# Performance work log

Measured on AMD Instinct MI355X. Metric: run time of the kernel, lower is better.

Reference implementation:

```python
import jax, jax.numpy as jnp
import numpy as np

D_MODEL = 256
D_FF = 2048
H_HEADS = 8
N_LEVELS = 5
N_POINTS = 4
SPATIAL = [(128, 128), (64, 64), (32, 32), (16, 16), (8, 8)]
LV = sum(h * w for h, w in SPATIAL)  # 21824
LQ = 900
B = 8
D_HEAD = D_MODEL // H_HEADS


def _layer_norm(x, g, b, eps=1e-5):
    m = jnp.mean(x, -1, keepdims=True)
    v = jnp.mean((x - m) ** 2, -1, keepdims=True)
    return (x - m) * jax.lax.rsqrt(v + eps) * g + b


def _ms_deform_core(value, loc, attn_w):
    # value [B,Lv,H,D]; loc [B,Lq,H,L,P,2] normalized in [0,1]; attn_w [B,Lq,H,L,P]
    Bn, Lq = loc.shape[0], loc.shape[1]
    Dh = value.shape[-1]
    out = jnp.zeros((Bn, H_HEADS, Lq, Dh), value.dtype)
    start = 0
    for l, (Hh, Ww) in enumerate(SPATIAL):
        v = value[:, start:start + Hh * Ww].transpose(0, 2, 1, 3)  # [B,H,HW,D]
        start += Hh * Ww
        xy = loc[:, :, :, l]  # [B,Lq,H,P,2]
        # grid_sample align_corners=False: pixel = norm*size - 0.5
        x = xy[..., 0] * Ww - 0.5
        y = xy[..., 1] * Hh - 0.5
        x0 = jnp.floor(x); y0 = jnp.floor(y)
        fx = x - x0; fy = y - y0
        samp = jnp.zeros((Bn, H_HEADS, Lq * N_POINTS, Dh), value.dtype)
        corners = ((0, 0, (1 - fx) * (1 - fy)), (1, 0, fx * (1 - fy)),
                   (0, 1, (1 - fx) * fy), (1, 1, fx * fy))
        for dx, dy, wgt in corners:
            xc = x0 + dx; yc = y0 + dy
            valid = (xc >= 0) & (xc < Ww) & (yc >= 0) & (yc < Hh)  # zero padding
            idx = (jnp.clip(yc, 0, Hh - 1) * Ww + jnp.clip(xc, 0, Ww - 1)).astype(jnp.int32)
            wv = jnp.where(valid, wgt, 0.0)
            idx_r = idx.transpose(0, 2, 1, 3).reshape(Bn, H_HEADS, Lq * N_POINTS)
            wv_r = wv.transpose(0, 2, 1, 3).reshape(Bn, H_HEADS, Lq * N_POINTS)
            g = jnp.take_along_axis(v, idx_r[..., None], axis=2)  # [B,H,LqP,D]
            samp = samp + wv_r[..., None] * g
        samp = samp.reshape(Bn, H_HEADS, Lq, N_POINTS, Dh)
        aw = attn_w[:, :, :, l].transpose(0, 2, 1, 3)  # [B,H,Lq,P]
        out = out + (samp * aw[..., None]).sum(axis=3)
    return out.transpose(0, 2, 1, 3).reshape(Bn, Lq, H_HEADS * Dh)


def _forward(tgt, tgt_query_pos, tgt_reference_points, memory,
             sa_w_q, sa_b_q, sa_w_k, sa_b_k, sa_w_v, sa_b_v, sa_w_o, sa_b_o,
             ca_w_off, ca_b_off, ca_w_attn, ca_b_attn, ca_w_val, ca_b_val, ca_w_out, ca_b_out,
             ffn_w1, ffn_b1, ffn_w2, ffn_b2,
             ln1_g, ln1_b, ln2_g, ln2_b, ln3_g, ln3_b):
    Lq, Bn, C = tgt.shape
    scale = float(1.0 / np.sqrt(D_HEAD))
    # ---- self-attention (torch nn.MultiheadAttention, seq-first) ----
    qk = tgt + tgt_query_pos
    def heads(x):
        return x.reshape(Lq, Bn, H_HEADS, D_HEAD).transpose(1, 2, 0, 3)
    q = heads(qk @ sa_w_q + sa_b_q) * scale
    k = heads(qk @ sa_w_k + sa_b_k)
    v = heads(tgt @ sa_w_v + sa_b_v)
    attn = jax.nn.softmax(jnp.einsum('bhqd,bhkd->bhqk', q, k), axis=-1)
    o = jnp.einsum('bhqk,bhkd->bhqd', attn, v).transpose(2, 0, 1, 3).reshape(Lq, Bn, C)
    tgt = _layer_norm(tgt + (o @ sa_w_o + sa_b_o), ln2_g, ln2_b)
    # ---- multi-scale deformable cross-attention ----
    qb = (tgt + tgt_query_pos).transpose(1, 0, 2)            # [B,Lq,C]
    ref = tgt_reference_points.transpose(1, 0, 2, 3)         # [B,Lq,L,2]
    value = (memory.transpose(1, 0, 2) @ ca_w_val + ca_b_val).reshape(Bn, LV, H_HEADS, D_HEAD)
    off = (qb @ ca_w_off + ca_b_off).reshape(Bn, Lq, H_HEADS, N_LEVELS, N_POINTS, 2)
    aw = jax.nn.softmax((qb @ ca_w_attn + ca_b_attn).reshape(Bn, Lq, H_HEADS, N_LEVELS * N_POINTS), axis=-1)
    aw = aw.reshape(Bn, Lq, H_HEADS, N_LEVELS, N_POINTS)
    offset_normalizer = jnp.asarray([[w, h] for h, w in SPATIAL], tgt.dtype)  # (W,H) per level
    loc = ref[:, :, None, :, None, :] + off / offset_normalizer[None, None, None, :, None, :]
    samp = _ms_deform_core(value, loc, aw)                   # [B,Lq,C]
    o = (samp @ ca_w_out + ca_b_out).transpose(1, 0, 2)
    tgt = _layer_norm(tgt + o, ln1_g, ln1_b)
    # ---- FFN ----
    h = jax.nn.relu(tgt @ ffn_w1 + ffn_b1)
    tgt = _layer_norm(tgt + (h @ ffn_w2 + ffn_b2), ln3_g, ln3_b)
    return tgt


def setup_inputs() -> dict:
    key = jax.random.key(0)
    ks = iter(jax.random.split(key, 64))
    f32 = jnp.float32
    def nrm(shape, s=1.0):
        return (s * jax.random.normal(next(ks), shape)).astype(f32)
    inp = {}
    inp['tgt'] = nrm((LQ, B, D_MODEL))
    inp['tgt_query_pos'] = nrm((LQ, B, D_MODEL))
    inp['tgt_reference_points'] = jax.random.uniform(next(ks), (LQ, B, N_LEVELS, 2), f32)
    inp['memory'] = nrm((LV, B, D_MODEL))
    inp['memory_spatial_shapes'] = jnp.asarray(SPATIAL, jnp.int32)
    inp['memory_level_start_index'] = jnp.asarray(np.cumsum([0] + [h * w for h, w in SPATIAL[:-1]]), jnp.int32)
    for n, shp in [('sa_w_q', (D_MODEL, D_MODEL)), ('sa_w_k', (D_MODEL, D_MODEL)),
                   ('sa_w_v', (D_MODEL, D_MODEL)), ('sa_w_o', (D_MODEL, D_MODEL)),
                   ('ca_w_off', (D_MODEL, H_HEADS * N_LEVELS * N_POINTS * 2)),
                   ('ca_w_attn', (D_MODEL, H_HEADS * N_LEVELS * N_POINTS)),
                   ('ca_w_val', (D_MODEL, D_MODEL)), ('ca_w_out', (D_MODEL, D_MODEL)),
                   ('ffn_w1', (D_MODEL, D_FF)), ('ffn_w2', (D_FF, D_MODEL))]:
        inp[n] = nrm(shp, 0.02)
    for n, d in [('sa_b_q', D_MODEL), ('sa_b_k', D_MODEL), ('sa_b_v', D_MODEL), ('sa_b_o', D_MODEL),
                 ('ca_b_off', H_HEADS * N_LEVELS * N_POINTS * 2), ('ca_b_attn', H_HEADS * N_LEVELS * N_POINTS),
                 ('ca_b_val', D_MODEL), ('ca_b_out', D_MODEL), ('ffn_b1', D_FF), ('ffn_b2', D_MODEL)]:
        inp[n] = jnp.zeros((d,), f32)
    for n in ['ln1', 'ln2', 'ln3']:
        inp[n + '_g'] = jnp.ones((D_MODEL,), f32)
        inp[n + '_b'] = jnp.zeros((D_MODEL,), f32)
    return inp


def reference(tgt, tgt_query_pos, tgt_reference_points, memory,
              memory_spatial_shapes, memory_level_start_index,
              sa_w_q, sa_b_q, sa_w_k, sa_b_k, sa_w_v, sa_b_v, sa_w_o, sa_b_o,
              ca_w_off, ca_b_off, ca_w_attn, ca_b_attn, ca_w_val, ca_b_val, ca_w_out, ca_b_out,
              ffn_w1, ffn_b1, ffn_w2, ffn_b2,
              ln1_g, ln1_b, ln2_g, ln2_b, ln3_g, ln3_b):
    # spatial shapes / level start index are static metadata (SPATIAL), kept for API parity
    return _forward(tgt, tgt_query_pos, tgt_reference_points, memory,
                    sa_w_q, sa_b_q, sa_w_k, sa_b_k, sa_w_v, sa_b_v, sa_w_o, sa_b_o,
                    ca_w_off, ca_b_off, ca_w_attn, ca_b_attn, ca_w_val, ca_b_val, ca_w_out, ca_b_out,
                    ffn_w1, ffn_b1, ffn_w2, ffn_b2,
                    ln1_g, ln1_b, ln2_g, ln2_b, ln3_g, ln3_b)
```

## Files before the change

kernel.cpp:

```cpp
#include <hip/hip_runtime.h>
#include <hip/hip_bf16.h>
#include <type_traits>

#define LQ    900
#define BSZ   8
#define ROWS  (LQ*BSZ)
#define CDIM  256
#define QKS   512
#define OAS   480
#define NH    8
#define DH    32
#define LVTOT 21824
#define VROWS (LVTOT*BSZ)
#define DFF   2048

typedef unsigned short u16;
typedef short short8 __attribute__((ext_vector_type(8)));
typedef float f32x4 __attribute__((ext_vector_type(4)));

__device__ __forceinline__ u16 f2bf(float f) {
    __hip_bfloat16 h = __float2bfloat16(f);
    return *reinterpret_cast<u16*>(&h);
}

#define SWZ(r) (((r) & 3) ^ (((r) >> 2) & 3))
#define ATTN_SCALE 0.1767766952966369f

struct PrepArgs {
    const float* Wq; const float* Wk; const float* Wv; const float* Wo;
    const float* Wval; const float* Wout; const float* Woff; const float* Watt;
    const float* W1; const float* W2;
    u16* WqkT; u16* WvT; u16* WoT; u16* WvalT; u16* WoutT; u16* WoaT; u16* W1T; u16* W2T;
    const float* bq; const float* bk; const float* boff; const float* batt;
    float* bqk; float* boa;
};
__global__ __launch_bounds__(256) void prep_kernel(PrepArgs a) {
    __shared__ float t[32][33];
    const int id = blockIdx.x;
    if (id == 1528) {
        const int tx = threadIdx.x;
        if (tx < 256) { a.bqk[tx] = a.bq[tx] * ATTN_SCALE; a.bqk[256 + tx] = a.bk[tx]; }
        for (int i = tx; i < 320; i += 256) a.boa[i] = a.boff[i];
        if (tx < 160) a.boa[320 + tx] = a.batt[tx];
        return;
    }
    const float* W; u16* Wt; int K = 256, N = 256, nx = 8; float scale = 1.f; int r;
    if      (id < 64)   { W = a.Wq;   Wt = a.WqkT;           scale = ATTN_SCALE; r = id; }
    else if (id < 128)  { W = a.Wk;   Wt = a.WqkT + 256*256; r = id - 64; }
    else if (id < 192)  { W = a.Wv;   Wt = a.WvT;            r = id - 128; }
    else if (id < 256)  { W = a.Wo;   Wt = a.WoT;            r = id - 192; }
    else if (id < 320)  { W = a.Wval; Wt = a.WvalT;          r = id - 256; }
    else if (id < 384)  { W = a.Wout; Wt = a.WoutT;          r = id - 320; }
    else if (id < 464)  { W = a.Woff; Wt = a.WoaT;           N = 320; nx = 10; r = id - 384; }
    else if (id < 504)  { W = a.Watt; Wt = a.WoaT + 320*256; N = 160; nx = 5;  r = id - 464; }
    else if (id < 1016) { W = a.W1;   Wt = a.W1T;            N = 2048; nx = 64; r = id - 504; }
    else                { W = a.W2;   Wt = a.W2T;            K = 2048; N = 256; nx = 8; r = id - 1016; }
    const int n0 = (r % nx) * 32, k0 = (r / nx) * 32;
    const int tx = threadIdx.x & 31, ty = threadIdx.x >> 5;
    #pragma unroll
    for (int rr = ty; rr < 32; rr += 8)
        t[rr][tx] = W[(size_t)(k0 + rr) * N + n0 + tx];
    __syncthreads();
    #pragma unroll
    for (int rr = ty; rr < 32; rr += 8)
        Wt[(size_t)(n0 + rr) * K + k0 + tx] = f2bf(t[tx][rr] * scale);
}

__device__ __forceinline__ void stage_lds(const u16* __restrict__ src, u16* dst,
                                          int row0, int K, int k0, int maxrow, int tid) {
    #pragma unroll
    for (int i = 0; i < 2; ++i) {
        const int gi = i*256 + tid;
        const int row = gi >> 2, c = gi & 3;
        int grow = row0 + row; if (grow > maxrow) grow = maxrow;
        const int sw = c ^ SWZ(row);
        const u16* gsrc = src + (size_t)grow * K + k0 + sw * 8;
        u16* ldst = dst + ((i*256 + (tid & 192)) << 3);
        __builtin_amdgcn_global_load_lds((const __attribute__((address_space(1))) void*)gsrc,
                                         (__attribute__((address_space(3))) void*)ldst, 16, 0, 0);
    }
}

__device__ __forceinline__ void load_A16r(float* f, const float* __restrict__ A,
                                          const float* __restrict__ A2,
                                          int arow, int K, int k0, int aoff) {
    const float4* src = reinterpret_cast<const float4*>(&A[(size_t)arow * K + k0 + aoff]);
    float4 v[4];
    #pragma unroll
    for (int i = 0; i < 4; ++i) v[i] = src[i];
    if (A2) {
        const float4* s2 = reinterpret_cast<const float4*>(&A2[(size_t)arow * K + k0 + aoff]);
        #pragma unroll
        for (int i = 0; i < 4; ++i) {
            float4 g = s2[i];
            v[i].x += g.x; v[i].y += g.y; v[i].z += g.z; v[i].w += g.w;
        }
    }
    #pragma unroll
    for (int i = 0; i < 4; ++i) {
        f[i*4+0] = v[i].x; f[i*4+1] = v[i].y; f[i*4+2] = v[i].z; f[i*4+3] = v[i].w;
    }
}

__device__ __forceinline__ void write_A16(u16* Adst, const float* f, int sr, int scb) {
    u16 t[16];
    #pragma unroll
    for (int i = 0; i < 16; ++i) t[i] = f2bf(f[i]);
    #pragma unroll
    for (int c4 = 0; c4 < 2; ++c4) {
        const int c = scb + c4;
        *reinterpret_cast<uint4*>(&Adst[sr*32 + ((c ^ SWZ(sr)) * 8)]) =
            *reinterpret_cast<const uint4*>(&t[c4*8]);
    }
}

__global__ __launch_bounds__(256) void mgemm3_kernel(
        const float* __restrict__ Aval, const u16* __restrict__ WvalT, const float* __restrict__ bval, u16* __restrict__ Cval,
        const float* __restrict__ Aqk,  const float* __restrict__ Aqk2, const u16* __restrict__ WqkT,
        const float* __restrict__ bqk,  u16* __restrict__ Cqk,
        const float* __restrict__ Av,   const u16* __restrict__ WvT,   const float* __restrict__ bv, u16* __restrict__ Cv) {
    __shared__ __align__(16) u16 S[16384];
    const int tid = threadIdx.x;
    int id = blockIdx.x;
    const float *A, *A2 = nullptr; const u16* Wt; const float* bias; u16* C; int M, N, bx, by;
    if (id < 2728)      { A = Aval; Wt = WvalT; bias = bval; C = Cval; M = VROWS; N = 256; bx = id & 1; by = id >> 1; }
    else if (id < 2956) { id -= 2728; A = Aqk; A2 = Aqk2; Wt = WqkT; bias = bqk; C = Cqk; M = ROWS; N = 512; bx = id & 3; by = id >> 2; }
    else                { id -= 2956; A = Av; Wt = WvT; bias = bv; C = Cv; M = ROWS; N = 256; bx = id & 1; by = id >> 1; }
    const int m0 = by * 128, n0 = bx * 128;
    const int lane = tid & 63;
    const int wr = (tid >> 7) & 1, wc = (tid >> 6) & 1;
    const int lr = lane & 15, lg = lane >> 4;
    const int sr = tid >> 1;
    const int scb = (tid & 1) * 2;
    const int aoff = scb * 8;
    const int arow = (m0 + sr < M) ? (m0 + sr) : (M - 1);

    f32x4 acc[4][4] = {};
    float fa[16];

    stage_lds(Wt, S + 8192, n0, 256, 0, N - 1, tid);
    load_A16r(fa, A, A2, arow, 256, 0, aoff);
    write_A16(S, fa, sr, scb);
    __syncthreads();

    #pragma unroll
    for (int t = 0; t < 8; ++t) {
        u16* Ac = S + ((t & 1) << 12);
        u16* Bc = S + 8192 + ((t & 1) << 12);
        const int nxt = (t + 1) & 1;
        if (t + 1 < 8) {
            stage_lds(Wt, S + 8192 + (nxt << 12), n0, 256, (t + 1) << 5, N - 1, tid);
            load_A16r(fa, A, A2, arow, 256, (t + 1) << 5, aoff);
        }
        short8 af[4], bfr[4];
        #pragma unroll
        for (int i = 0; i < 4; ++i) {
            const int r = wr*64 + i*16 + lr;
            af[i] = *reinterpret_cast<const short8*>(&Ac[r*32 + ((lg ^ SWZ(r)) * 8)]);
        }
        #pragma unroll
        for (int j = 0; j < 4; ++j) {
            const int r = wc*64 + j*16 + lr;
            bfr[j] = *reinterpret_cast<const short8*>(&Bc[r*32 + ((lg ^ SWZ(r)) * 8)]);
        }
        #pragma unroll
        for (int i = 0; i < 4; ++i)
            #pragma unroll
            for (int j = 0; j < 4; ++j)
                acc[i][j] = __builtin_amdgcn_mfma_f32_16x16x32_bf16(af[i], bfr[j], acc[i][j], 0, 0, 0);
        if (t + 1 < 8)
            write_A16(S + (nxt << 12), fa, sr, scb);
        __syncthreads();
    }

    u16* Ct = S;
    #pragma unroll
    for (int j = 0; j < 4; ++j) {
        const int col = wc*64 + j*16 + lr;
        const float bcol = bias[n0 + col];
        #pragma unroll
        for (int i = 0; i < 4; ++i)
            #pragma unroll
            for (int r = 0; r < 4; ++r)
                Ct[(wr*64 + i*16 + lg*4 + r)*128 + col] = f2bf(acc[i][j][r] + bcol);
    }
    __syncthreads();
    #pragma unroll
    for (int it = 0; it < 8; ++it) {
        const int idx = it*256 + tid;
        const int row = idx >> 4, cc = idx & 15;
        if (m0 + row < M)
            *reinterpret_cast<uint4*>(&C[(size_t)(m0 + row) * N + n0 + cc*8]) =
                *reinterpret_cast<const uint4*>(&Ct[row*128 + cc*8]);
    }
}

template<typename AT, int RELU, int ADD, typename OutT>
__global__ __launch_bounds__(256) void gemm_mfma(const AT* __restrict__ A,
                                                 const float* __restrict__ A2,
                                                 const u16* __restrict__ Wt,
                                                 const float* __restrict__ bias,
                                                 OutT* __restrict__ C,
                                                 int M, int N, int K) {
    __shared__ __align__(16) u16 S[16384];
    const int tid = threadIdx.x;
    const int m0 = blockIdx.y * 128, n0 = blockIdx.x * 128;
    const int lane = tid & 63;
    const int wr = (tid >> 7) & 1, wc = (tid >> 6) & 1;
    const int lr = lane & 15, lg = lane >> 4;
    const int sr = tid >> 1;
    const int scb = (tid & 1) * 2;
    const int aoff = scb * 8;
    const int nsteps = K >> 5;
    const int arow = (m0 + sr < M) ? (m0 + sr) : (M - 1);

    f32x4 acc[4][4] = {};
    float fa[16];

    stage_lds(Wt, S + 8192, n0, K, 0, N - 1, tid);
    if constexpr (std::is_same<AT, float>::value) {
        load_A16r(fa, A, ADD ? A2 : nullptr, arow, K, 0, aoff);
        write_A16(S, fa, sr, scb);
    } else {
        stage_lds((const u16*)A, S, m0, K, 0, M - 1, tid);
    }
    __syncthreads();

    for (int t = 0; t < nsteps; ++t) {
        u16* Ac = S + ((t & 1) << 12);
        u16* Bc = S + 8192 + ((t & 1) << 12);
        const int nxt = (t + 1) & 1;
        if (t + 1 < nsteps) {
            stage_lds(Wt, S + 8192 + (nxt << 12), n0, K, (t + 1) << 5, N - 1, tid);
            if constexpr (std::is_same<AT, float>::value)
                load_A16r(fa, A, ADD ? A2 : nullptr, arow, K, (t + 1) << 5, aoff);
            else
                stage_lds((const u16*)A, S + (nxt << 12), m0, K, (t + 1) << 5, M - 1, tid);
        }
        short8 af[4], bfr[4];
        #pragma unroll
        for (int i = 0; i < 4; ++i) {
            const int r = wr*64 + i*16 + lr;
            af[i] = *reinterpret_cast<const short8*>(&Ac[r*32 + ((lg ^ SWZ(r)) * 8)]);
        }
        #pragma unroll
        for (int j = 0; j < 4; ++j) {
            const int r = wc*64 + j*16 + lr;
            bfr[j] = *reinterpret_cast<const short8*>(&Bc[r*32 + ((lg ^ SWZ(r)) * 8)]);
        }
        #pragma unroll
        for (int i = 0; i < 4; ++i)
            #pragma unroll
            for (int j = 0; j < 4; ++j)
                acc[i][j] = __builtin_amdgcn_mfma_f32_16x16x32_bf16(af[i], bfr[j], acc[i][j], 0, 0, 0);
        if (t + 1 < nsteps) {
            if constexpr (std::is_same<AT, float>::value)
                write_A16(S + (nxt << 12), fa, sr, scb);
        }
        __syncthreads();
    }

    if constexpr (std::is_same<OutT, float>::value) {
        #pragma unroll
        for (int j = 0; j < 4; ++j) {
            const int col = n0 + wc*64 + j*16 + lr;
            if (col >= N) continue;
            const float bcol = bias[col];
            #pragma unroll
            for (int i = 0; i < 4; ++i) {
                #pragma unroll
                for (int r = 0; r < 4; ++r) {
                    const int row = m0 + wr*64 + i*16 + lg*4 + r;
                    if (row >= M) continue;
                    float v = acc[i][j][r] + bcol;
                    if (RELU) v = fmaxf(v, 0.f);
                    C[(size_t)row * N + col] = v;
                }
            }
        }
    } else {
        u16* Ct = S;
        #pragma unroll
        for (int j = 0; j < 4; ++j) {
            const int col = wc*64 + j*16 + lr;
            const float bcol = bias[n0 + col];
            #pragma unroll
            for (int i = 0; i < 4; ++i)
                #pragma unroll
                for (int r = 0; r < 4; ++r) {
                    float v = acc[i][j][r] + bcol;
                    if (RELU) v = fmaxf(v, 0.f);
                    Ct[(wr*64 + i*16 + lg*4 + r)*128 + col] = f2bf(v);
                }
        }
        __syncthreads();
        #pragma unroll
        for (int it = 0; it < 8; ++it) {
            const int idx = it*256 + tid;
            const int row = idx >> 4, cc = idx & 15;
            if (m0 + row < M)
                *reinterpret_cast<uint4*>(&C[(size_t)(m0 + row) * N + n0 + cc*8]) =
                    *reinterpret_cast<const uint4*>(&Ct[row*128 + cc*8]);
        }
    }
}

__global__ __launch_bounds__(256) void attn_mfma_kernel(const u16* __restrict__ qkb,
                                                        const u16* __restrict__ vb,
                                                        float* __restrict__ out) {
    __shared__ __align__(16) u16 Ks[64*32];
    __shared__ __align__(16) u16 Vt[32*64];
    const int bx = blockIdx.x;
    const int qt = bx & 7, h = (bx >> 3) & 7, b = bx >> 6;
    const int tid = threadIdx.x;
    const int w = tid >> 6, lane = tid & 63;
    const int lr = lane & 15, lg = lane >> 4;
    const int m0 = qt*128 + w*32;

    short8 qf[2];
    #pragma unroll
    for (int j = 0; j < 2; ++j) {
        int lq = m0 + j*16 + lr; if (lq > LQ-1) lq = LQ-1;
        qf[j] = *reinterpret_cast<const short8*>(&qkb[((size_t)lq*BSZ + b)*QKS + h*DH + lg*8]);
    }

    f32x4 o00 = {}, o01 = {}, o10 = {}, o11 = {};
    float m[2] = {-1e30f, -1e30f}, l[2] = {0.f, 0.f};
    const f32x4 zero = {};

    for (int kt = 0; kt < 15; ++kt) {
        __syncthreads();
        {
            const int key = tid >> 2, c = tid & 3;
            int kg = kt*64 + key; if (kg > LQ-1) kg = LQ-1;
            *reinterpret_cast<short8*>(&Ks[key*32 + ((c ^ ((key>>1)&3)) * 8)]) =
                *reinterpret_cast<const short8*>(&qkb[((size_t)kg*BSZ + b)*QKS + 256 + h*DH + c*8]);
            short8 vv = *reinterpret_cast<const short8*>(&vb[((size_t)kg*BSZ + b)*CDIM + h*DH + c*8]);
            const u16* pv = reinterpret_cast<const u16*>(&vv);
            #pragma unroll
            for (int e = 0; e < 8; ++e) {
                const int dh = c*8 + e;
                Vt[dh*64 + (((key>>3) ^ (dh&7)) * 8) + (key&7)] = pv[e];
            }
        }
        __syncthreads();

        f32x4 s[4][2];
        #pragma unroll
        for (int i = 0; i < 4; ++i) {
            const int key = i*16 + lr;
            short8 kf = *reinterpret_cast<const short8*>(&Ks[key*32 + ((lg ^ ((key>>1)&3)) * 8)]);
            s[i][0] = __builtin_amdgcn_mfma_f32_16x16x32_bf16(kf, qf[0], zero, 0, 0, 0);
            s[i][1] = __builtin_amdgcn_mfma_f32_16x16x32_bf16(kf, qf[1], zero, 0, 0, 0);
        }
        const int lim = LQ - kt*64 - lg*4;
        #pragma unroll
        for (int i = 0; i < 4; ++i)
            #pragma unroll
            for (int r = 0; r < 4; ++r)
                if (i*16 + r >= lim) { s[i][0][r] = -1e30f; s[i][1][r] = -1e30f; }

        #pragma unroll
        for (int j = 0; j < 2; ++j) {
            float mx = -1e30f;
            #pragma unroll
            for (int i = 0; i < 4; ++i)
                #pragma unroll
                for (int r = 0; r < 4; ++r) mx = fmaxf(mx, s[i][j][r]);
            mx = fmaxf(mx, __shfl_xor(mx, 16));
            mx = fmaxf(mx, __shfl_xor(mx, 32));
            const float mn = fmaxf(m[j], mx);
            const float corr = __expf(m[j] - mn);
            float sum = 0.f;
            #pragma unroll
            for (int i = 0; i < 4; ++i)
                #pragma unroll
                for (int r = 0; r < 4; ++r) {
                    float p = __expf(s[i][j][r] - mn);
                    s[i][j][r] = p;
                    sum += p;
                }
            sum += __shfl_xor(sum, 16);
            sum += __shfl_xor(sum, 32);
            l[j] = l[j]*corr + sum;
            m[j] = mn;
            if (j == 0) { o00 *= corr; o10 *= corr; }
            else        { o01 *= corr; o11 *= corr; }
        }

        short8 pb[2][2];
        #pragma unroll
        for (int kh = 0; kh < 2; ++kh)
            #pragma unroll
            for (int j = 0; j < 2; ++j) {
                u16 t[8];
                #pragma unroll
                for (int e = 0; e < 4; ++e) {
                    t[e]   = f2bf(s[2*kh][j][e]);
                    t[e+4] = f2bf(s[2*kh+1][j][e]);
                }
                pb[kh][j] = *reinterpret_cast<short8*>(t);
            }

        #pragma unroll
        for (int ip = 0; ip < 2; ++ip) {
            const int dh = ip*16 + lr;
            #pragma unroll
            for (int kh = 0; kh < 2; ++kh) {
                u16 t[8];
                const int c0 = (kh*4 + (lg>>1)) ^ (dh&7);
                const int c1 = (kh*4 + 2 + (lg>>1)) ^ (dh&7);
                *reinterpret_cast<uint2*>(&t[0]) =
                    *reinterpret_cast<const uint2*>(&Vt[dh*64 + c0*8 + (lg&1)*4]);
                *reinterpret_cast<uint2*>(&t[4]) =
                    *reinterpret_cast<const uint2*>(&Vt[dh*64 + c1*8 + (lg&1)*4]);
                short8 vf = *reinterpret_cast<short8*>(t);
                if (ip == 0) {
                    o00 = __builtin_amdgcn_mfma_f32_16x16x32_bf16(vf, pb[kh][0], o00, 0, 0, 0);
                    o01 = __builtin_amdgcn_mfma_f32_16x16x32_bf16(vf, pb[kh][1], o01, 0, 0, 0);
                } else {
                    o10 = __builtin_amdgcn_mfma_f32_16x16x32_bf16(vf, pb[kh][0], o10, 0, 0, 0);
                    o11 = __builtin_amdgcn_mfma_f32_16x16x32_bf16(vf, pb[kh][1], o11, 0, 0, 0);
                }
            }
        }
    }

    #pragma unroll
    for (int j = 0; j < 2; ++j) {
        const int lq = m0 + j*16 + lr;
        if (lq >= LQ) continue;
        const float inv = 1.f / l[j];
        float* op = &out[((size_t)lq*BSZ + b)*CDIM + h*DH];
        #pragma unroll
        for (int r = 0; r < 4; ++r) {
            const f32x4& a0 = (j == 0) ? o00 : o01;
            const f32x4& a1 = (j == 0) ? o10 : o11;
            op[lg*4 + r]      = a0[r] * inv;
            op[16 + lg*4 + r] = a1[r] * inv;
        }
    }
}

__global__ __launch_bounds__(256) void ln_res_kernel(const float* __restrict__ xin,
                                                     const float* __restrict__ res,
                                                     const float* __restrict__ g,
                                                     const float* __restrict__ beta,
                                                     float* __restrict__ out) {
    const int row  = blockIdx.x * 4 + (threadIdx.x >> 6);
    const int lane = threadIdx.x & 63;
    const size_t base = (size_t)row * CDIM + lane * 4;
    float4 a = *reinterpret_cast<const float4*>(&xin[base]);
    float4 r = *reinterpret_cast<const float4*>(&res[base]);
    float x0 = a.x+r.x, x1 = a.y+r.y, x2 = a.z+r.z, x3 = a.w+r.w;
    float s = x0+x1+x2+x3;
    #pragma unroll
    for (int o = 1; o < 64; o <<= 1) s += __shfl_xor(s, o);
    float mean = s * (1.f/256.f);
    float d0 = x0-mean, d1 = x1-mean, d2 = x2-mean, d3 = x3-mean;
    float sq = d0*d0 + d1*d1 + d2*d2 + d3*d3;
    #pragma unroll
    for (int o = 1; o < 64; o <<= 1) sq += __shfl_xor(sq, o);
    float rs = rsqrtf(sq * (1.f/256.f) + 1e-5f);
    float4 gg = *reinterpret_cast<const float4*>(&g[lane*4]);
    float4 bb = *reinterpret_cast<const float4*>(&beta[lane*4]);
    float4 o4 = make_float4(d0*rs*gg.x+bb.x, d1*rs*gg.y+bb.y, d2*rs*gg.z+bb.z, d3*rs*gg.w+bb.w);
    *reinterpret_cast<float4*>(&out[base]) = o4;
}

__global__ __launch_bounds__(256) void softmax20_kernel(float* __restrict__ oab) {
    int item = blockIdx.x * 256 + threadIdx.x;
    if (item >= ROWS * NH) return;
    int row = item >> 3, h = item & 7;
    float* p = &oab[(size_t)row*OAS + 320 + h*20];
    float mx = -1e30f;
    float e[20];
    #pragma unroll
    for (int j = 0; j < 20; ++j) mx = fmaxf(mx, p[j]);
    float sum = 0.f;
    #pragma unroll
    for (int j = 0; j < 20; ++j) { e[j] = __expf(p[j] - mx); sum += e[j]; }
    float inv = 1.f / sum;
    #pragma unroll
    for (int j = 0; j < 20; ++j) p[j] = e[j] * inv;
}

__global__ __launch_bounds__(256) void msdeform_kernel(const u16* __restrict__ value,
                                                       const float* __restrict__ oab,
                                                       const float* __restrict__ refp,
                                                       float* __restrict__ samp) {
    const int gid = blockIdx.x * 32 + (threadIdx.x >> 3);
    const int ch  = (threadIdx.x & 7) * 4;
    const int h   = gid & 7;
    const int row = gid >> 3;
    const int b   = row & 7;
    const int WL[5] = {128, 64, 32, 16, 8};
    const int SL[5] = {0, 16384, 20480, 21504, 21760};
    const u16* vbase = value + h*DH + ch;
    float a0 = 0.f, a1 = 0.f, a2 = 0.f, a3 = 0.f;
    #pragma unroll
    for (int l = 0; l < 5; ++l) {
        const float2 r2 = *reinterpret_cast<const float2*>(&refp[((size_t)row*5 + l)*2]);
        const int W = WL[l];
        const float Wf = (float)W;
        #pragma unroll
        for (int p = 0; p < 4; ++p) {
            const float2 o2 = *reinterpret_cast<const float2*>(&oab[(size_t)row*OAS + ((h*5 + l)*4 + p)*2]);
            const float aw = oab[(size_t)row*OAS + 320 + h*20 + l*4 + p];
            const float x = (r2.x + o2.x / Wf) * Wf - 0.5f;
            const float y = (r2.y + o2.y / Wf) * Wf - 0.5f;
            const float x0f = floorf(x), y0f = floorf(y);
            const float fx = x - x0f, fy = y - y0f;
            const int x0 = (int)x0f, y0 = (int)y0f;
            float wx0 = (1.f - fx) * aw, wx1 = fx * aw;
            float fy0 = 1.f - fy, fy1 = fy;
            if (x0 < 0 || x0 >= W)       wx0 = 0.f;
            if (x0+1 < 0 || x0+1 >= W)   wx1 = 0.f;
            if (y0 < 0 || y0 >= W)       fy0 = 0.f;
            if (y0+1 < 0 || y0+1 >= W)   fy1 = 0.f;
            const float w00 = wx0*fy0, w10 = wx1*fy0, w01 = wx0*fy1, w11 = wx1*fy1;
            const int xc0 = min(max(x0, 0), W-1),   xc1 = min(max(x0+1, 0), W-1);
            const int yc0 = min(max(y0, 0), W-1),   yc1 = min(max(y0+1, 0), W-1);
            const int r0 = SL[l] + yc0*W, r1 = SL[l] + yc1*W;
            const int o00i = ((r0 + xc0)*BSZ + b) * CDIM;
            const int o10i = ((r0 + xc1)*BSZ + b) * CDIM;
            const int o01i = ((r1 + xc0)*BSZ + b) * CDIM;
            const int o11i = ((r1 + xc1)*BSZ + b) * CDIM;
            const uint2 u00 = *reinterpret_cast<const uint2*>(vbase + o00i);
            const uint2 u10 = *reinterpret_cast<const uint2*>(vbase + o10i);
            const uint2 u01 = *reinterpret_cast<const uint2*>(vbase + o01i);
            const uint2 u11 = *reinterpret_cast<const uint2*>(vbase + o11i);
            a0 += w00 * __uint_as_float(u00.x << 16) + w10 * __uint_as_float(u10.x << 16)
                + w01 * __uint_as_float(u01.x << 16) + w11 * __uint_as_float(u11.x << 16);
            a1 += w00 * __uint_as_float(u00.x & 0xffff0000u) + w10 * __uint_as_float(u10.x & 0xffff0000u)
                + w01 * __uint_as_float(u01.x & 0xffff0000u) + w11 * __uint_as_float(u11.x & 0xffff0000u);
            a2 += w00 * __uint_as_float(u00.y << 16) + w10 * __uint_as_float(u10.y << 16)
                + w01 * __uint_as_float(u01.y << 16) + w11 * __uint_as_float(u11.y << 16);
            a3 += w00 * __uint_as_float(u00.y & 0xffff0000u) + w10 * __uint_as_float(u10.y & 0xffff0000u)
                + w01 * __uint_as_float(u01.y & 0xffff0000u) + w11 * __uint_as_float(u11.y & 0xffff0000u);
        }
    }
    float4 o4 = make_float4(a0, a1, a2, a3);
    *reinterpret_cast<float4*>(&samp[(size_t)row*CDIM + h*DH + ch]) = o4;
}

extern "C" void kernel_launch(void* const* d_in, const int* in_sizes, int n_in,
                              void* d_out, int out_size, void* d_ws, size_t ws_size,
                              hipStream_t stream) {
    (void)in_sizes; (void)n_in; (void)out_size; (void)ws_size;
    const float* tgt    = (const float*)d_in[0];
    const float* qpos   = (const float*)d_in[1];
    const float* refpts = (const float*)d_in[2];
    const float* memory = (const float*)d_in[3];
    const float* Wq  = (const float*)d_in[6];
    const float* Wk  = (const float*)d_in[7];
    const float* Wv  = (const float*)d_in[8];
    const float* Wo  = (const float*)d_in[9];
    const float* Woff= (const float*)d_in[10];
    const float* Watt= (const float*)d_in[11];
    const float* Wval= (const float*)d_in[12];
    const float* Wout= (const float*)d_in[13];
    const float* W1  = (const float*)d_in[14];
    const float* W2  = (const float*)d_in[15];
    const float* bq  = (const float*)d_in[16];
    const float* bk  = (const float*)d_in[17];
    const float* bv  = (const float*)d_in[18];
    const float* bo  = (const float*)d_in[19];
    const float* boff= (const float*)d_in[20];
    const float* batt= (const float*)d_in[21];
    const float* bval= (const float*)d_in[22];
    const float* bout= (const float*)d_in[23];
    const float* b1  = (const float*)d_in[24];
    const float* b2  = (const float*)d_in[25];
    const float* ln1g= (const float*)d_in[26];
    const float* ln1b= (const float*)d_in[27];
    const float* ln2g= (const float*)d_in[28];
    const float* ln2b= (const float*)d_in[29];
    const float* ln3g= (const float*)d_in[30];
    const float* ln3b= (const float*)d_in[31];
    float* out = (float*)d_out;

    char* ws = (char*)d_ws;
    const size_t RB = (size_t)ROWS * CDIM * 4;
    float* tgt2  = (float*)(ws + 0*RB);
    float* tgt3  = (float*)(ws + 1*RB);
    float* qk    = (float*)(ws + 2*RB);
    float* vbuf  = (float*)(ws + 3*RB);
    float* abuf  = (float*)(ws + 4*RB);
    u16* qkb = (u16*)(ws + 5*RB);
    u16* vb  = (u16*)(ws + 5*RB + (size_t)ROWS*QKS*2);
    float* oab = (float*)(ws + 5*RB + (size_t)ROWS*QKS*2 + (size_t)ROWS*CDIM*2);
    char* wsm = ws + 5*RB + (size_t)ROWS*QKS*2 + (size_t)ROWS*CDIM*2 + (size_t)ROWS*OAS*4;
    u16* WqkT  = (u16*)(wsm);
    u16* WvT   = (u16*)(wsm + 262144);
    u16* WoT   = (u16*)(wsm + 262144 + 1*131072);
    u16* WvalT = (u16*)(wsm + 262144 + 2*131072);
    u16* WoutT = (u16*)(wsm + 262144 + 3*131072);
    u16* WoaT  = (u16*)(wsm + 262144 + 4*131072);
    u16* W1T   = (u16*)(wsm + 2*262144 + 4*131072);
    u16* W2T   = (u16*)(wsm + 2*262144 + 4*131072 + 1048576);
    float* bqk = (float*)(wsm + 2*262144 + 4*131072 + 2097152);
    float* boa = (float*)(wsm + 2*262144 + 4*131072 + 2097152 + 2048);
    char* big  = wsm + 2*262144 + 4*131072 + 2097152 + 4096;
    u16* valb  = (u16*)big;
    u16* ffnh  = (u16*)(big + (size_t)VROWS*CDIM*2);

    const dim3 blk(256);

    PrepArgs pa = { Wq, Wk, Wv, Wo, Wval, Wout, Woff, Watt, W1, W2,
                    WqkT, WvT, WoT, WvalT, WoutT, WoaT, W1T, W2T,
                    bq, bk, boff, batt, bqk, boa };
    prep_kernel<<<dim3(1529), blk, 0, stream>>>(pa);

    mgemm3_kernel<<<dim3(3070), blk, 0, stream>>>(
        memory, WvalT, bval, valb,
        tgt, qpos, WqkT, bqk, qkb,
        tgt, WvT, bv, vb);

    attn_mfma_kernel<<<dim3(512), blk, 0, stream>>>(qkb, vb, abuf);
    gemm_mfma<float,0,0,float><<<dim3(2,57), blk, 0, stream>>>(abuf, nullptr, WoT, bo, qk, ROWS, CDIM, CDIM);
    ln_res_kernel<<<dim3(ROWS/4), blk, 0, stream>>>(qk, tgt, ln2g, ln2b, tgt2);

    gemm_mfma<float,0,1,float><<<dim3(4,57), blk, 0, stream>>>(tgt2, qpos, WoaT, boa, oab, ROWS, OAS, CDIM);
    softmax20_kernel<<<dim3((ROWS*NH+255)/256), blk, 0, stream>>>(oab);
    msdeform_kernel<<<dim3(ROWS*NH/32), blk, 0, stream>>>(valb, oab, refpts, vbuf);
    gemm_mfma<float,0,0,float><<<dim3(2,57), blk, 0, stream>>>(vbuf, nullptr, WoutT, bout, qk, ROWS, CDIM, CDIM);
    ln_res_kernel<<<dim3(ROWS/4), blk, 0, stream>>>(qk, tgt2, ln1g, ln1b, tgt3);

    gemm_mfma<float,1,0,u16><<<dim3(16,57), blk, 0, stream>>>(tgt3, nullptr, W1T, b1, ffnh, ROWS, DFF, CDIM);
    gemm_mfma<u16,0,0,float><<<dim3(2,57),  blk, 0, stream>>>(ffnh, nullptr, W2T, b2, abuf, ROWS, CDIM, DFF);
    ln_res_kernel<<<dim3(ROWS/4), blk, 0, stream>>>(abuf, tgt3, ln3g, ln3b, out);
}
```

Measured before the change: 358.2 us.

## Replace LDS-staged GEMMs with direct global-to-register MFMA fragment loads

After: 487.9 us. 1.36x slower.

```diff
diff --git a/kernel.cpp b/kernel.cpp
--- a/kernel.cpp
+++ b/kernel.cpp
@@ -22,8 +22,6 @@
     __hip_bfloat16 h = __float2bfloat16(f);
     return *reinterpret_cast<u16*>(&h);
 }
-
-#define SWZ(r) (((r) & 3) ^ (((r) >> 2) & 3))
 #define ATTN_SCALE 0.1767766952966369f
 
 struct PrepArgs {
@@ -66,198 +64,98 @@
         Wt[(size_t)(n0 + rr) * K + k0 + tx] = f2bf(t[tx][rr] * scale);
 }
 
-__device__ __forceinline__ void stage_lds(const u16* __restrict__ src, u16* dst,
-                                          int row0, int K, int k0, int maxrow, int tid) {
-    #pragma unroll
-    for (int i = 0; i < 2; ++i) {
-        const int gi = i*256 + tid;
-        const int row = gi >> 2, c = gi & 3;
-        int grow = row0 + row; if (grow > maxrow) grow = maxrow;
-        const int sw = c ^ SWZ(row);
-        const u16* gsrc = src + (size_t)grow * K + k0 + sw * 8;
-        u16* ldst = dst + ((i*256 + (tid & 192)) << 3);
-        __builtin_amdgcn_global_load_lds((const __attribute__((address_space(1))) void*)gsrc,
-                                         (__attribute__((address_space(3))) void*)ldst, 16, 0, 0);
-    }
-}
-
-__device__ __forceinline__ void load_A16r(float* f, const float* __restrict__ A,
-                                          const float* __restrict__ A2,
-                                          int arow, int K, int k0, int aoff) {
-    const float4* src = reinterpret_cast<const float4*>(&A[(size_t)arow * K + k0 + aoff]);
-    float4 v[4];
-    #pragma unroll
-    for (int i = 0; i < 4; ++i) v[i] = src[i];
-    if (A2) {
-        const float4* s2 = reinterpret_cast<const float4*>(&A2[(size_t)arow * K + k0 + aoff]);
-        #pragma unroll
-        for (int i = 0; i < 4; ++i) {
-            float4 g = s2[i];
-            v[i].x += g.x; v[i].y += g.y; v[i].z += g.z; v[i].w += g.w;
-        }
-    }
-    #pragma unroll
-    for (int i = 0; i < 4; ++i) {
-        f[i*4+0] = v[i].x; f[i*4+1] = v[i].y; f[i*4+2] = v[i].z; f[i*4+3] = v[i].w;
-    }
-}
-
-__device__ __forceinline__ void write_A16(u16* Adst, const float* f, int sr, int scb) {
-    u16 t[16];
-    #pragma unroll
-    for (int i = 0; i < 16; ++i) t[i] = f2bf(f[i]);
-    #pragma unroll
-    for (int c4 = 0; c4 < 2; ++c4) {
-        const int c = scb + c4;
-        *reinterpret_cast<uint4*>(&Adst[sr*32 + ((c ^ SWZ(sr)) * 8)]) =
-            *reinterpret_cast<const uint4*>(&t[c4*8]);
-    }
-}
-
-__global__ __launch_bounds__(256) void mgemm3_kernel(
-        const float* __restrict__ Aval, const u16* __restrict__ WvalT, const float* __restrict__ bval, u16* __restrict__ Cval,
-        const float* __restrict__ Aqk,  const float* __restrict__ Aqk2, const u16* __restrict__ WqkT,
-        const float* __restrict__ bqk,  u16* __restrict__ Cqk,
-        const float* __restrict__ Av,   const u16* __restrict__ WvT,   const float* __restrict__ bv, u16* __restrict__ Cv) {
-    __shared__ __align__(16) u16 S[16384];
-    const int tid = threadIdx.x;
-    int id = blockIdx.x;
-    const float *A, *A2 = nullptr; const u16* Wt; const float* bias; u16* C; int M, N, bx, by;
-    if (id < 2728)      { A = Aval; Wt = WvalT; bias = bval; C = Cval; M = VROWS; N = 256; bx = id & 1; by = id >> 1; }
-    else if (id < 2956) { id -= 2728; A = Aqk; A2 = Aqk2; Wt = WqkT; bias = bqk; C = Cqk; M = ROWS; N = 512; bx = id & 3; by = id >> 2; }
-    else                { id -= 2956; A = Av; Wt = WvT; bias = bv; C = Cv; M = ROWS; N = 256; bx = id & 1; by = id >> 1; }
-    const int m0 = by * 128, n0 = bx * 128;
+__device__ __forceinline__ short8 cvt8(float4 lo, float4 hi) {
+    u16 t[8] = { f2bf(lo.x), f2bf(lo.y), f2bf(lo.z), f2bf(lo.w),
+                 f2bf(hi.x), f2bf(hi.y), f2bf(hi.z), f2bf(hi.w) };
+    return *reinterpret_cast<short8*>(t);
+}
+
+template<typename AT, int RELU, int ADD, typename OutT>
+__device__ __forceinline__ void gemm_body(const AT* __restrict__ A, const float* __restrict__ A2,
+                                          const u16* __restrict__ Wt, const float* __restrict__ bias,
+                                          OutT* __restrict__ C, int M, int N, int K,
+                                          int m0, int n0, int tid) {
+    extern __shared__ u16 Sep[];
     const int lane = tid & 63;
     const int wr = (tid >> 7) & 1, wc = (tid >> 6) & 1;
     const int lr = lane & 15, lg = lane >> 4;
-    const int sr = tid >> 1;
-    const int scb = (tid & 1) * 2;
-    const int aoff = scb * 8;
-    const int arow = (m0 + sr < M) ? (m0 + sr) : (M - 1);
-
+    int trow[4], ncol[4];
+    #pragma unroll
+    for (int i = 0; i < 4; ++i) {
+        int r = m0 + wr*64 + i*16 + lr;
+        trow[i] = (r < M) ? r : (M - 1);
+        ncol[i] = n0 + wc*64 + i*16 + lr;
+    }
     f32x4 acc[4][4] = {};
-    float fa[16];
-
-    stage_lds(Wt, S + 8192, n0, 256, 0, N - 1, tid);
-    load_A16r(fa, A, A2, arow, 256, 0, aoff);
-    write_A16(S, fa, sr, scb);
-    __syncthreads();
-
-    #pragma unroll
-    for (int t = 0; t < 8; ++t) {
-        u16* Ac = S + ((t & 1) << 12);
-        u16* Bc = S + 8192 + ((t & 1) << 12);
-        const int nxt = (t + 1) & 1;
-        if (t + 1 < 8) {
-            stage_lds(Wt, S + 8192 + (nxt << 12), n0, 256, (t + 1) << 5, N - 1, tid);
-            load_A16r(fa, A, A2, arow, 256, (t + 1) << 5, aoff);
-        }
-        short8 af[4], bfr[4];
-        #pragma unroll
-        for (int i = 0; i < 4; ++i) {
-            const int r = wr*64 + i*16 + lr;
-            af[i] = *reinterpret_cast<const short8*>(&Ac[r*32 + ((lg ^ SWZ(r)) * 8)]);
-        }
-        #pragma unroll
-        for (int j = 0; j < 4; ++j) {
-            const int r = wc*64 + j*16 + lr;
-            bfr[j] = *reinterpret_cast<const short8*>(&Bc[r*32 + ((lg ^ SWZ(r)) * 8)]);
-        }
-        #pragma unroll
-        for (int i = 0; i < 4; ++i)
+    const int ns = K >> 5;
+
+    if constexpr (std::is_same<AT, float>::value) {
+        float4 a0[4][2], a1[4][2], p0[4][2], p1[4][2];
+        short8 b0[4], b1[4];
+        auto issue = [&](float4 (&aa)[4][2], float4 (&pp)[4][2], short8 (&bb)[4], int k0) {
+            #pragma unroll
+            for (int i = 0; i < 4; ++i) {
+                const float* p = &A[(size_t)trow[i]*K + k0 + lg*8];
+                aa[i][0] = *reinterpret_cast<const float4*>(p);
+                aa[i][1] = *reinterpret_cast<const float4*>(p + 4);
+                if constexpr (ADD) {
+                    const float* q = &A2[(size_t)trow[i]*K + k0 + lg*8];
+                    pp[i][0] = *reinterpret_cast<const float4*>(q);
+                    pp[i][1] = *reinterpret_cast<const float4*>(q + 4);
+                }
+            }
             #pragma unroll
             for (int j = 0; j < 4; ++j)
-                acc[i][j] = __builtin_amdgcn_mfma_f32_16x16x32_bf16(af[i], bfr[j], acc[i][j], 0, 0, 0);
-        if (t + 1 < 8)
-            write_A16(S + (nxt << 12), fa, sr, scb);
-        __syncthreads();
-    }
-
-    u16* Ct = S;
-    #pragma unroll
-    for (int j = 0; j < 4; ++j) {
-        const int col = wc*64 + j*16 + lr;
-        const float bcol = bias[n0 + col];
-        #pragma unroll
-        for (int i = 0; i < 4; ++i)
-            #pragma unroll
-            for (int r = 0; r < 4; ++r)
-                Ct[(wr*64 + i*16 + lg*4 + r)*128 + col] = f2bf(acc[i][j][r] + bcol);
-    }
-    __syncthreads();
-    #pragma unroll
-    for (int it = 0; it < 8; ++it) {
-        const int idx = it*256 + tid;
-        const int row = idx >> 4, cc = idx & 15;
-        if (m0 + row < M)
-            *reinterpret_cast<uint4*>(&C[(size_t)(m0 + row) * N + n0 + cc*8]) =
-                *reinterpret_cast<const uint4*>(&Ct[row*128 + cc*8]);
-    }
-}
-
-template<typename AT, int RELU, int ADD, typename OutT>
-__global__ __launch_bounds__(256) void gemm_mfma(const AT* __restrict__ A,
-                                                 const float* __restrict__ A2,
-                                                 const u16* __restrict__ Wt,
-                                                 const float* __restrict__ bias,
-                                                 OutT* __restrict__ C,
-                                                 int M, int N, int K) {
-    __shared__ __align__(16) u16 S[16384];
-    const int tid = threadIdx.x;
-    const int m0 = blockIdx.y * 128, n0 = blockIdx.x * 128;
-    const int lane = tid & 63;
-    const int wr = (tid >> 7) & 1, wc = (tid >> 6) & 1;
-    const int lr = lane & 15, lg = lane >> 4;
-    const int sr = tid >> 1;
-    const int scb = (tid & 1) * 2;
-    const int aoff = scb * 8;
-    const int nsteps = K >> 5;
-    const int arow = (m0 + sr < M) ? (m0 + sr) : (M - 1);
-
-    f32x4 acc[4][4] = {};
-    float fa[16];
-
-    stage_lds(Wt, S + 8192, n0, K, 0, N - 1, tid);
-    if constexpr (std::is_same<AT, float>::value) {
-        load_A16r(fa, A, ADD ? A2 : nullptr, arow, K, 0, aoff);
-        write_A16(S, fa, sr, scb);
+                bb[j] = *reinterpret_cast<const short8*>(&Wt[(size_t)ncol[j]*K + k0 + lg*8]);
+        };
+        auto comp = [&](float4 (&aa)[4][2], float4 (&pp)[4][2], short8 (&bb)[4]) {
+            short8 af[4];
+            #pragma unroll
+            for (int i = 0; i < 4; ++i) {
+                float4 lo = aa[i][0], hi = aa[i][1];
+                if constexpr (ADD) {
+                    lo.x += pp[i][0].x; lo.y += pp[i][0].y; lo.z += pp[i][0].z; lo.w += pp[i][0].w;
+                    hi.x += pp[i][1].x; hi.y += pp[i][1].y; hi.z += pp[i][1].z; hi.w += pp[i][1].w;
+                }
+                af[i] = cvt8(lo, hi);
+            }
+            #pragma unroll
+            for (int i = 0; i < 4; ++i)
+                #pragma unroll
+                for (int j = 0; j < 4; ++j)
+                    acc[i][j] = __builtin_amdgcn_mfma_f32_16x16x32_bf16(af[i], bb[j], acc[i][j], 0, 0, 0);
+        };
+        issue(a0, p0, b0, 0);
+        for (int t = 0; t < ns; t += 2) {
+            issue(a1, p1, b1, (t + 1) << 5);
+            comp(a0, p0, b0);
+            if (t + 2 < ns) issue(a0, p0, b0, (t + 2) << 5);
+            comp(a1, p1, b1);
+        }
     } else {
-        stage_lds((const u16*)A, S, m0, K, 0, M - 1, tid);
-    }
-    __syncthreads();
-
-    for (int t = 0; t < nsteps; ++t) {
-        u16* Ac = S + ((t & 1) << 12);
-        u16* Bc = S + 8192 + ((t & 1) << 12);
-        const int nxt = (t + 1) & 1;
-        if (t + 1 < nsteps) {
-            stage_lds(Wt, S + 8192 + (nxt << 12), n0, K, (t + 1) << 5, N - 1, tid);
-            if constexpr (std::is_same<AT, float>::value)
-                load_A16r(fa, A, ADD ? A2 : nullptr, arow, K, (t + 1) << 5, aoff);
-            else
-                stage_lds((const u16*)A, S + (nxt << 12), m0, K, (t + 1) << 5, M - 1, tid);
-        }
-        short8 af[4], bfr[4];
-        #pragma unroll
-        for (int i = 0; i < 4; ++i) {
-            const int r = wr*64 + i*16 + lr;
-            af[i] = *reinterpret_cast<const short8*>(&Ac[r*32 + ((lg ^ SWZ(r)) * 8)]);
-        }
-        #pragma unroll
-        for (int j = 0; j < 4; ++j) {
-            const int r = wc*64 + j*16 + lr;
-            bfr[j] = *reinterpret_cast<const short8*>(&Bc[r*32 + ((lg ^ SWZ(r)) * 8)]);
-        }
-        #pragma unroll
-        for (int i = 0; i < 4; ++i)
+        short8 a0[4], a1[4], b0[4], b1[4];
+        auto issue = [&](short8 (&aa)[4], short8 (&bb)[4], int k0) {
+            #pragma unroll
+            for (int i = 0; i < 4; ++i)
+                aa[i] = *reinterpret_cast<const short8*>(&((const u16*)A)[(size_t)trow[i]*K + k0 + lg*8]);
             #pragma unroll
             for (int j = 0; j < 4; ++j)
-                acc[i][j] = __builtin_amdgcn_mfma_f32_16x16x32_bf16(af[i], bfr[j], acc[i][j], 0, 0, 0);
-        if (t + 1 < nsteps) {
-            if constexpr (std::is_same<AT, float>::value)
-                write_A16(S + (nxt << 12), fa, sr, scb);
-        }
-        __syncthreads();
+                bb[j] = *reinterpret_cast<const short8*>(&Wt[(size_t)ncol[j]*K + k0 + lg*8]);
+        };
+        auto comp = [&](short8 (&aa)[4], short8 (&bb)[4]) {
+            #pragma unroll
+            for (int i = 0; i < 4; ++i)
+                #pragma unroll
+                for (int j = 0; j < 4; ++j)
+                    acc[i][j] = __builtin_amdgcn_mfma_f32_16x16x32_bf16(aa[i], bb[j], acc[i][j], 0, 0, 0);
+        };
+        issue(a0, b0, 0);
+        for (int t = 0; t < ns; t += 2) {
+            issue(a1, b1, (t + 1) << 5);
+            comp(a0, b0);
+            if (t + 2 < ns) issue(a0, b0, (t + 2) << 5);
+            comp(a1, b1);
+        }
     }
 
     if constexpr (std::is_same<OutT, float>::value) {
@@ -279,7 +177,7 @@
             }
         }
     } else {
-        u16* Ct = S;
+        __syncthreads();
         #pragma unroll
         for (int j = 0; j < 4; ++j) {
             const int col = wc*64 + j*16 + lr;
@@ -290,7 +188,7 @@
                 for (int r = 0; r < 4; ++r) {
                     float v = acc[i][j][r] + bcol;
                     if (RELU) v = fmaxf(v, 0.f);
-                    Ct[(wr*64 + i*16 + lg*4 + r)*128 + col] = f2bf(v);
+                    Sep[(wr*64 + i*16 + lg*4 + r)*128 + col] = f2bf(v);
                 }
         }
         __syncthreads();
@@ -300,8 +198,36 @@
             const int row = idx >> 4, cc = idx & 15;
             if (m0 + row < M)
                 *reinterpret_cast<uint4*>(&C[(size_t)(m0 + row) * N + n0 + cc*8]) =
-                    *reinterpret_cast<const uint4*>(&Ct[row*128 + cc*8]);
-        }
+                    *reinterpret_cast<const uint4*>(&Sep[row*128 + cc*8]);
+        }
+    }
+}
+
+template<typename AT, int RELU, int ADD, typename OutT>
+__global__ __launch_bounds__(256) void gemm_direct(const AT* __restrict__ A, const float* __restrict__ A2,
+                                                   const u16* __restrict__ Wt, const float* __restrict__ bias,
+                                                   OutT* __restrict__ C, int M, int N, int K) {
+    gemm_body<AT, RELU, ADD, OutT>(A, A2, Wt, bias, C, M, N, K,
+                                   blockIdx.y * 128, blockIdx.x * 128, threadIdx.x);
+}
+
+__global__ __launch_bounds__(256) void mgemm3_kernel(
+        const float* __restrict__ Aval, const u16* __restrict__ WvalT, const float* __restrict__ bval, u16* __restrict__ Cval,
+        const float* __restrict__ Aqk,  const float* __restrict__ Aqk2, const u16* __restrict__ WqkT,
+        const float* __restrict__ bqk,  u16* __restrict__ Cqk,
+        const float* __restrict__ Av,   const u16* __restrict__ WvT,   const float* __restrict__ bv, u16* __restrict__ Cv) {
+    int id = blockIdx.x;
+    if (id < 2728) {
+        gemm_body<float,0,0,u16>(Aval, nullptr, WvalT, bval, Cval, VROWS, 256, 256,
+                                 (id >> 1) * 128, (id & 1) * 128, threadIdx.x);
+    } else if (id < 2956) {
+        id -= 2728;
+        gemm_body<float,0,1,u16>(Aqk, Aqk2, WqkT, bqk, Cqk, ROWS, 512, 256,
+                                 (id >> 2) * 128, (id & 3) * 128, threadIdx.x);
+    } else {
+        id -= 2956;
+        gemm_body<float,0,0,u16>(Av, nullptr, WvT, bv, Cv, ROWS, 256, 256,
+                                 (id >> 1) * 128, (id & 1) * 128, threadIdx.x);
     }
 }
 
@@ -612,22 +538,22 @@
                     bq, bk, boff, batt, bqk, boa };
     prep_kernel<<<dim3(1529), blk, 0, stream>>>(pa);
 
-    mgemm3_kernel<<<dim3(3070), blk, 0, stream>>>(
+    mgemm3_kernel<<<dim3(3070), blk, 32768, stream>>>(
         memory, WvalT, bval, valb,
         tgt, qpos, WqkT, bqk, qkb,
         tgt, WvT, bv, vb);
 
     attn_mfma_kernel<<<dim3(512), blk, 0, stream>>>(qkb, vb, abuf);
-    gemm_mfma<float,0,0,float><<<dim3(2,57), blk, 0, stream>>>(abuf, nullptr, WoT, bo, qk, ROWS, CDIM, CDIM);
+    gemm_direct<float,0,0,float><<<dim3(2,57), blk, 0, stream>>>(abuf, nullptr, WoT, bo, qk, ROWS, CDIM, CDIM);
     ln_res_kernel<<<dim3(ROWS/4), blk, 0, stream>>>(qk, tgt, ln2g, ln2b, tgt2);
 
-    gemm_mfma<float,0,1,float><<<dim3(4,57), blk, 0, stream>>>(tgt2, qpos, WoaT, boa, oab, ROWS, OAS, CDIM);
+    gemm_direct<float,0,1,float><<<dim3(4,57), blk, 0, stream>>>(tgt2, qpos, WoaT, boa, oab, ROWS, OAS, CDIM);
     softmax20_kernel<<<dim3((ROWS*NH+255)/256), blk, 0, stream>>>(oab);
     msdeform_kernel<<<dim3(ROWS*NH/32), blk, 0, stream>>>(valb, oab, refpts, vbuf);
-    gemm_mfma<float,0,0,float><<<dim3(2,57), blk, 0, stream>>>(vbuf, nullptr, WoutT, bout, qk, ROWS, CDIM, CDIM);
+    gemm_direct<float,0,0,float><<<dim3(2,57), blk, 0, stream>>>(vbuf, nullptr, WoutT, bout, qk, ROWS, CDIM, CDIM);
     ln_res_kernel<<<dim3(ROWS/4), blk, 0, stream>>>(qk, tgt2, ln1g, ln1b, tgt3);
 
-    gemm_mfma<float,1,0,u16><<<dim3(16,57), blk, 0, stream>>>(tgt3, nullptr, W1T, b1, ffnh, ROWS, DFF, CDIM);
-    gemm_mfma<u16,0,0,float><<<dim3(2,57),  blk, 0, stream>>>(ffnh, nullptr, W2T, b2, abuf, ROWS, CDIM, DFF);
+    gemm_direct<float,1,0,u16><<<dim3(16,57), blk, 32768, stream>>>(tgt3, nullptr, W1T, b1, ffnh, ROWS, DFF, CDIM);
+    gemm_direct<u16,0,0,float><<<dim3(2,57),  blk, 0, stream>>>(ffnh, nullptr, W2T, b2, abuf, ROWS, CDIM, DFF);
     ln_res_kernel<<<dim3(ROWS/4), blk, 0, stream>>>(abuf, tgt3, ln3g, ln3b, out);
 }
```
